# Performance work log

Measured on AMD Instinct MI355X. Metric: run time of the kernel, lower is better.

## Reference

```python
import jax, jax.numpy as jnp
import numpy as np

MARGIN = 0.3

def _cdist(x):
    # pairwise euclidean distances, safe sqrt (zero grad at 0)
    sq = jnp.sum(x * x, axis=1)
    d2 = sq[:, None] + sq[None, :] - 2.0 * (x @ x.T)
    d2 = jnp.maximum(d2, 0.0)
    safe = jnp.where(d2 > 0, d2, 1.0)
    return jnp.where(d2 > 0, jnp.sqrt(safe), 0.0)

def setup_inputs() -> dict:
    key = jax.random.key(0)
    k1, k2 = jax.random.split(key)
    embeddings = jax.random.normal(k1, (4096, 128), dtype=jnp.float32)
    labels = jax.random.randint(k2, (4096,), 0, 256)
    return {"embeddings": embeddings, "labels": labels}

def reference(embeddings, labels):
    B = embeddings.shape[0]
    dist = _cdist(embeddings)                      # [B, B]
    same = labels[:, None] == labels[None, :]      # [B, B]
    eye = jnp.eye(B, dtype=bool)
    pos_mask = same & ~eye
    neg_mask = ~same
    neg_inf = jnp.array(-jnp.inf, dist.dtype)
    pos_inf = jnp.array(jnp.inf, dist.dtype)
    hard_pos = jnp.max(jnp.where(pos_mask, dist, neg_inf), axis=1)  # [B]
    hard_neg = jnp.min(jnp.where(neg_mask, dist, pos_inf), axis=1)  # [B]
    valid = jnp.any(pos_mask, axis=1) & jnp.any(neg_mask, axis=1)
    per_row = jax.nn.relu(hard_pos - hard_neg + MARGIN)
    per_row = jnp.where(valid, per_row, 0.0)
    num_valid = jnp.sum(valid.astype(dist.dtype))
    return jnp.sum(per_row) / jnp.maximum(num_valid, 1.0)
```

## Files before the change

kernel.cpp:

```cpp
#include <hip/hip_runtime.h>
#include <hip/hip_bf16.h>


typedef __attribute__((ext_vector_type(8))) short short8;
typedef __attribute__((ext_vector_type(4))) float f32x4;

#define MARGIN_F 0.3f
#define WST 72

__device__ inline unsigned short f2bf(float x) {
    __hip_bfloat16 h = __float2bfloat16(x);
    return *(unsigned short*)&h;
}
__device__ inline float bf2f(unsigned short u) {
    __hip_bfloat16 h;
    *(unsigned short*)&h = u;
    return __bfloat162float(h);
}

__global__ __launch_bounds__(256) void tl_prep(const float* __restrict__ E,
                                               unsigned short* __restrict__ Ecat,
                                               float* __restrict__ sqn,
                                               unsigned* __restrict__ hpb,
                                               unsigned* __restrict__ hnb) {
    int t = blockIdx.x * 256 + threadIdx.x;
    int row = t >> 5;
    int kq = (t & 31) * 4;
    float4 v = *(const float4*)&E[(size_t)row * 128 + kq];
    float s = fmaf(v.x, v.x, fmaf(v.y, v.y, fmaf(v.z, v.z, v.w * v.w)));

    unsigned short hx = f2bf(v.x), hy = f2bf(v.y), hz = f2bf(v.z), hw = f2bf(v.w);
    unsigned short lx = f2bf(v.x - bf2f(hx)), ly = f2bf(v.y - bf2f(hy));
    unsigned short lz = f2bf(v.z - bf2f(hz)), lw = f2bf(v.w - bf2f(hw));
    ushort4 hi4; hi4.x = hx; hi4.y = hy; hi4.z = hz; hi4.w = hw;
    ushort4 lo4; lo4.x = lx; lo4.y = ly; lo4.z = lz; lo4.w = lw;
    *(ushort4*)&Ecat[(size_t)row * 256 + kq] = hi4;
    *(ushort4*)&Ecat[(size_t)row * 256 + 128 + kq] = lo4;

#pragma unroll
    for (int m = 1; m < 32; m <<= 1) s += __shfl_xor(s, m);
    if ((t & 31) == 0) {
        sqn[row] = s;
        hpb[row] = 0u;
        hnb[row] = 0x7F800000u;
    }
}

__global__ __launch_bounds__(256) void tl_phase1(const unsigned short* __restrict__ Ecat,
                                                 const int* __restrict__ labels,
                                                 const float* __restrict__ sqn,
                                                 unsigned* __restrict__ hpb,
                                                 unsigned* __restrict__ hnb) {
    __shared__ unsigned short Al[128 * WST];
    __shared__ unsigned short Bl[128 * WST];
    const int tid = threadIdx.x;
    const int l = tid & 63, w = tid >> 6;
    const int wr = w >> 1, wc = w & 1;
    const int q = l >> 4, r16 = l & 15;
    const int i0 = blockIdx.x * 128;
    const int jgrp = blockIdx.y * 256;

    float mp[4][4], mn[4][4];
    int li[4][4];
    float si[4][4];
#pragma unroll
    for (int ti = 0; ti < 4; ++ti)
#pragma unroll
        for (int p = 0; p < 4; ++p) {
            mp[ti][p] = 0.0f;
            mn[ti][p] = 3.4e38f;
            int rrow = i0 + wr * 64 + ti * 16 + q * 4 + p;
            li[ti][p] = labels[rrow];
            si[ti][p] = sqn[rrow];
        }

    for (int js = 0; js < 2; ++js) {
        const int jb = jgrp + js * 128;
        f32x4 acc[4][4];
#pragma unroll
        for (int ti = 0; ti < 4; ++ti)
#pragma unroll
            for (int tj = 0; tj < 4; ++tj) acc[ti][tj] = (f32x4)0.0f;

        for (int kc = 0; kc < 4; ++kc) {
            __syncthreads();
#pragma unroll
            for (int it = 0; it < 4; ++it) {
                int idx = it * 256 + tid;
                int rr = idx >> 3, ko = (idx & 7) * 8;
                *(short8*)&Al[rr * WST + ko] =
                    *(const short8*)&Ecat[(size_t)(i0 + rr) * 256 + kc * 64 + ko];
                *(short8*)&Bl[rr * WST + ko] =
                    *(const short8*)&Ecat[(size_t)(jb + rr) * 256 + kc * 64 + ko];
            }
            __syncthreads();
#pragma unroll
            for (int s = 0; s < 2; ++s) {
                short8 af[4], bf[4];
#pragma unroll
                for (int t2 = 0; t2 < 4; ++t2) {
                    af[t2] = *(const short8*)&Al[(wr * 64 + t2 * 16 + r16) * WST + s * 32 + q * 8];
                    bf[t2] = *(const short8*)&Bl[(wc * 64 + t2 * 16 + r16) * WST + s * 32 + q * 8];
                }
#pragma unroll
                for (int ti = 0; ti < 4; ++ti)
#pragma unroll
                    for (int tj = 0; tj < 4; ++tj)
                        acc[ti][tj] = __builtin_amdgcn_mfma_f32_16x16x32_bf16(
                            af[ti], bf[tj], acc[ti][tj], 0, 0, 0);
            }
        }
#pragma unroll
        for (int tj = 0; tj < 4; ++tj) {
            int cj = jb + wc * 64 + tj * 16 + r16;
            int ljv = labels[cj];
            float sjv = sqn[cj];
#pragma unroll
            for (int ti = 0; ti < 4; ++ti) {
#pragma unroll
                for (int p = 0; p < 4; ++p) {
                    float g = acc[ti][tj][p];
                    float d2 = fmaf(-2.0f, g, si[ti][p] + sjv);
                    d2 = fmaxf(d2, 0.0f);
                    int rrow = i0 + wr * 64 + ti * 16 + q * 4 + p;
                    bool same = (li[ti][p] == ljv);
                    bool posok = same && (rrow != cj);
                    mp[ti][p] = fmaxf(mp[ti][p], posok ? d2 : 0.0f);
                    mn[ti][p] = fminf(mn[ti][p], same ? 3.4e38f : d2);
                }
            }
        }
    }
#pragma unroll
    for (int ti = 0; ti < 4; ++ti)
#pragma unroll
        for (int p = 0; p < 4; ++p) {
            float a = mp[ti][p], b = mn[ti][p];
#pragma unroll
            for (int m = 1; m < 16; m <<= 1) {
                a = fmaxf(a, __shfl_xor(a, m));
                b = fminf(b, __shfl_xor(b, m));
            }
            if (r16 == 0) {
                int rrow = i0 + wr * 64 + ti * 16 + q * 4 + p;
                atomicMax(&hpb[rrow], __float_as_uint(a));
                atomicMin(&hnb[rrow], __float_as_uint(b));
            }
        }
}

__global__ __launch_bounds__(1024) void tl_phase2(const int* __restrict__ labels,
                                                  const unsigned* __restrict__ hpb,
                                                  const unsigned* __restrict__ hnb,
                                                  float* __restrict__ out) {
    __shared__ unsigned hist[256];
    __shared__ float sp[16], sv[16];
    int tid = threadIdx.x;
    if (tid < 256) hist[tid] = 0u;
    __syncthreads();
#pragma unroll
    for (int k = 0; k < 4; ++k) atomicAdd(&hist[labels[tid + k * 1024]], 1u);
    __syncthreads();
    float sum = 0.0f, nv = 0.0f;
#pragma unroll
    for (int k = 0; k < 4; ++k) {
        int r = tid + k * 1024;
        unsigned cnt = hist[labels[r]];
        bool valid = (cnt >= 2u) && (cnt < 4096u);
        float hp = sqrtf(__uint_as_float(hpb[r]));
        float hn = sqrtf(__uint_as_float(hnb[r]));
        float pr = fmaxf(hp - hn + MARGIN_F, 0.0f);
        if (valid) { sum += pr; nv += 1.0f; }
    }
#pragma unroll
    for (int m = 1; m < 64; m <<= 1) {
        sum += __shfl_xor(sum, m);
        nv += __shfl_xor(nv, m);
    }
    int wv = tid >> 6;
    if ((tid & 63) == 0) { sp[wv] = sum; sv[wv] = nv; }
    __syncthreads();
    if (tid == 0) {
        float ts = 0.0f, tn = 0.0f;
#pragma unroll
        for (int i = 0; i < 16; ++i) { ts += sp[i]; tn += sv[i]; }
        out[0] = ts / fmaxf(tn, 1.0f);
    }
}

extern "C" void kernel_launch(void* const* d_in, const int* in_sizes, int n_in,
                              void* d_out, int out_size, void* d_ws, size_t ws_size,
                              hipStream_t stream) {
    const float* E = (const float*)d_in[0];
    const int* labels = (const int*)d_in[1];
    float* out = (float*)d_out;

    unsigned short* Ecat = (unsigned short*)d_ws;
    char* base = (char*)d_ws + (size_t)4096 * 256 * 2;
    float* sqn = (float*)base;
    unsigned* hpb = (unsigned*)(base + 16384);
    unsigned* hnb = (unsigned*)(base + 32768);

    tl_prep<<<512, 256, 0, stream>>>(E, Ecat, sqn, hpb, hnb);
    tl_phase1<<<dim3(32, 16), 256, 0, stream>>>(Ecat, labels, sqn, hpb, hnb);
    tl_phase2<<<1, 1024, 0, stream>>>(labels, hpb, hnb, out);
}
```

Measured before the change: 88.15 us.

## Exploit distance-matrix symmetry by computing only upper-triangular tiles

Phase 1 now launches one block per upper-triangular 128x128 tile pair (528 blocks) instead of covering the full matrix with 512 blocks of 128x256. Each off-diagonal tile updates both the row and the column hardest-positive/negative via extra column reductions and atomics. Diagonal tiles reuse the A tile in shared memory as B. This roughly halves the MFMA and load work, at the cost of index math, more atomics and a shorter per-block workload.

Measured after the change: 86.84 us. Within noise of the previous version (-1.5%).

```diff
diff --git a/kernel.cpp b/kernel.cpp
--- a/kernel.cpp
+++ b/kernel.cpp
@@ -53,16 +53,23 @@
                                                  unsigned* __restrict__ hnb) {
     __shared__ unsigned short Al[128 * WST];
     __shared__ unsigned short Bl[128 * WST];
+
+    const int t = blockIdx.x;
+    int bi = (int)((65.0f - sqrtf(4225.0f - 8.0f * (float)t)) * 0.5f);
+    bi = min(max(bi, 0), 31);
+    while (bi < 31 && ((bi + 1) * (65 - (bi + 1))) / 2 <= t) ++bi;
+    while (bi > 0 && (bi * (65 - bi)) / 2 > t) --bi;
+    const int bj = bi + (t - (bi * (65 - bi)) / 2);
+    const bool diag = (bi == bj);
+    const int i0 = bi * 128, j0 = bj * 128;
+
     const int tid = threadIdx.x;
     const int l = tid & 63, w = tid >> 6;
     const int wr = w >> 1, wc = w & 1;
     const int q = l >> 4, r16 = l & 15;
-    const int i0 = blockIdx.x * 128;
-    const int jgrp = blockIdx.y * 256;
-
-    float mp[4][4], mn[4][4];
+
+    float mp[4][4], mn[4][4], si[4][4];
     int li[4][4];
-    float si[4][4];
 #pragma unroll
     for (int ti = 0; ti < 4; ++ti)
 #pragma unroll
@@ -74,60 +81,73 @@
             si[ti][p] = sqn[rrow];
         }
 
-    for (int js = 0; js < 2; ++js) {
-        const int jb = jgrp + js * 128;
-        f32x4 acc[4][4];
-#pragma unroll
-        for (int ti = 0; ti < 4; ++ti)
-#pragma unroll
-            for (int tj = 0; tj < 4; ++tj) acc[ti][tj] = (f32x4)0.0f;
-
-        for (int kc = 0; kc < 4; ++kc) {
-            __syncthreads();
-#pragma unroll
-            for (int it = 0; it < 4; ++it) {
-                int idx = it * 256 + tid;
-                int rr = idx >> 3, ko = (idx & 7) * 8;
-                *(short8*)&Al[rr * WST + ko] =
-                    *(const short8*)&Ecat[(size_t)(i0 + rr) * 256 + kc * 64 + ko];
+    f32x4 acc[4][4];
+#pragma unroll
+    for (int ti = 0; ti < 4; ++ti)
+#pragma unroll
+        for (int tj = 0; tj < 4; ++tj) acc[ti][tj] = (f32x4)0.0f;
+
+    const unsigned short* Bsel = diag ? Al : Bl;
+
+    for (int kc = 0; kc < 4; ++kc) {
+        __syncthreads();
+#pragma unroll
+        for (int it = 0; it < 4; ++it) {
+            int idx = it * 256 + tid;
+            int rr = idx >> 3, ko = (idx & 7) * 8;
+            *(short8*)&Al[rr * WST + ko] =
+                *(const short8*)&Ecat[(size_t)(i0 + rr) * 256 + kc * 64 + ko];
+            if (!diag)
                 *(short8*)&Bl[rr * WST + ko] =
-                    *(const short8*)&Ecat[(size_t)(jb + rr) * 256 + kc * 64 + ko];
-            }
-            __syncthreads();
-#pragma unroll
-            for (int s = 0; s < 2; ++s) {
-                short8 af[4], bf[4];
-#pragma unroll
-                for (int t2 = 0; t2 < 4; ++t2) {
-                    af[t2] = *(const short8*)&Al[(wr * 64 + t2 * 16 + r16) * WST + s * 32 + q * 8];
-                    bf[t2] = *(const short8*)&Bl[(wc * 64 + t2 * 16 + r16) * WST + s * 32 + q * 8];
-                }
-#pragma unroll
-                for (int ti = 0; ti < 4; ++ti)
-#pragma unroll
-                    for (int tj = 0; tj < 4; ++tj)
-                        acc[ti][tj] = __builtin_amdgcn_mfma_f32_16x16x32_bf16(
-                            af[ti], bf[tj], acc[ti][tj], 0, 0, 0);
-            }
-        }
-#pragma unroll
-        for (int tj = 0; tj < 4; ++tj) {
-            int cj = jb + wc * 64 + tj * 16 + r16;
-            int ljv = labels[cj];
-            float sjv = sqn[cj];
-#pragma unroll
-            for (int ti = 0; ti < 4; ++ti) {
-#pragma unroll
-                for (int p = 0; p < 4; ++p) {
-                    float g = acc[ti][tj][p];
-                    float d2 = fmaf(-2.0f, g, si[ti][p] + sjv);
-                    d2 = fmaxf(d2, 0.0f);
-                    int rrow = i0 + wr * 64 + ti * 16 + q * 4 + p;
-                    bool same = (li[ti][p] == ljv);
-                    bool posok = same && (rrow != cj);
-                    mp[ti][p] = fmaxf(mp[ti][p], posok ? d2 : 0.0f);
-                    mn[ti][p] = fminf(mn[ti][p], same ? 3.4e38f : d2);
-                }
+                    *(const short8*)&Ecat[(size_t)(j0 + rr) * 256 + kc * 64 + ko];
+        }
+        __syncthreads();
+#pragma unroll
+        for (int s = 0; s < 2; ++s) {
+            short8 af[4], bf[4];
+#pragma unroll
+            for (int t2 = 0; t2 < 4; ++t2) {
+                af[t2] = *(const short8*)&Al[(wr * 64 + t2 * 16 + r16) * WST + s * 32 + q * 8];
+                bf[t2] = *(const short8*)&Bsel[(wc * 64 + t2 * 16 + r16) * WST + s * 32 + q * 8];
+            }
+#pragma unroll
+            for (int ti = 0; ti < 4; ++ti)
+#pragma unroll
+                for (int tj = 0; tj < 4; ++tj)
+                    acc[ti][tj] = __builtin_amdgcn_mfma_f32_16x16x32_bf16(
+                        af[ti], bf[tj], acc[ti][tj], 0, 0, 0);
+        }
+    }
+
+#pragma unroll
+    for (int tj = 0; tj < 4; ++tj) {
+        int cj = j0 + wc * 64 + tj * 16 + r16;
+        int ljv = labels[cj];
+        float sjv = sqn[cj];
+        float cMP = 0.0f, cMN = 3.4e38f;
+#pragma unroll
+        for (int ti = 0; ti < 4; ++ti) {
+#pragma unroll
+            for (int p = 0; p < 4; ++p) {
+                float g = acc[ti][tj][p];
+                float d2 = fmaxf(fmaf(-2.0f, g, si[ti][p] + sjv), 0.0f);
+                bool same = (li[ti][p] == ljv);
+                int rrow = i0 + wr * 64 + ti * 16 + q * 4 + p;
+                bool self = diag && (rrow == cj);
+                mp[ti][p] = fmaxf(mp[ti][p], (same && !self) ? d2 : 0.0f);
+                mn[ti][p] = fminf(mn[ti][p], same ? 3.4e38f : d2);
+                cMP = fmaxf(cMP, same ? d2 : 0.0f);
+                cMN = fminf(cMN, same ? 3.4e38f : d2);
+            }
+        }
+        if (!diag) {
+            cMP = fmaxf(cMP, __shfl_xor(cMP, 16));
+            cMP = fmaxf(cMP, __shfl_xor(cMP, 32));
+            cMN = fminf(cMN, __shfl_xor(cMN, 16));
+            cMN = fminf(cMN, __shfl_xor(cMN, 32));
+            if (l < 16) {
+                atomicMax(&hpb[cj], __float_as_uint(cMP));
+                atomicMin(&hnb[cj], __float_as_uint(cMN));
             }
         }
     }
@@ -202,6 +222,6 @@
     unsigned* hnb = (unsigned*)(base + 32768);
 
     tl_prep<<<512, 256, 0, stream>>>(E, Ecat, sqn, hpb, hnb);
-    tl_phase1<<<dim3(32, 16), 256, 0, stream>>>(Ecat, labels, sqn, hpb, hnb);
+    tl_phase1<<<528, 256, 0, stream>>>(Ecat, labels, sqn, hpb, hnb);
     tl_phase2<<<1, 1024, 0, stream>>>(labels, hpb, hnb, out);
 }
```

## Use direct global-to-LDS loads with XOR swizzle, split tiles, and drop atomics

Applied to the files above, without the earlier changes.

Phase 1 now gives each block a single 128x128 tile on a 32x32 grid, up from two column tiles per block. It loads operands with global_load_lds into an XOR-swizzled LDS layout instead of going through registers into a padded layout. The per-row sqn add and the self-index comparison move out of the inner epilogue, and per-tile partial max/min are written to scratch buffers instead of global atomics. Phase 2 runs on 16 blocks that reduce these partials and combine results through an atomic counter. The aim is more parallelism, cheaper staging and a shorter epilogue, at the cost of extra partial-buffer traffic and a more complex final reduction.

Measured after the change: 82.17 us. 1.07x faster.

```diff
diff --git a/kernel.cpp b/kernel.cpp
--- a/kernel.cpp
+++ b/kernel.cpp
@@ -6,24 +6,32 @@
 typedef __attribute__((ext_vector_type(4))) float f32x4;
 
 #define MARGIN_F 0.3f
-#define WST 72
+#define NEG_BIG -3.4e38f
+#define POS_BIG 3.4e38f
+
+__device__ __forceinline__ void gl_lds16(const void* g, void* l) {
+    __builtin_amdgcn_global_load_lds(
+        (const __attribute__((address_space(1))) void*)g,
+        (__attribute__((address_space(3))) void*)l, 16, 0, 0);
+}
 
 __device__ inline unsigned short f2bf(float x) {
-    __hip_bfloat16 h = __float2bfloat16(x);
-    return *(unsigned short*)&h;
+    union { __hip_bfloat16 h; unsigned short u; } c;
+    c.h = __float2bfloat16(x);
+    return c.u;
 }
 __device__ inline float bf2f(unsigned short u) {
-    __hip_bfloat16 h;
-    *(unsigned short*)&h = u;
-    return __bfloat162float(h);
+    union { __hip_bfloat16 h; unsigned short us; } c;
+    c.us = u;
+    return __bfloat162float(c.h);
 }
 
 __global__ __launch_bounds__(256) void tl_prep(const float* __restrict__ E,
                                                unsigned short* __restrict__ Ecat,
                                                float* __restrict__ sqn,
-                                               unsigned* __restrict__ hpb,
-                                               unsigned* __restrict__ hnb) {
+                                               unsigned* __restrict__ accum) {
     int t = blockIdx.x * 256 + threadIdx.x;
+    if (t < 4) accum[t] = 0u;
     int row = t >> 5;
     int kq = (t & 31) * 4;
     float4 v = *(const float4*)&E[(size_t)row * 128 + kq];
@@ -39,97 +47,92 @@
 
 #pragma unroll
     for (int m = 1; m < 32; m <<= 1) s += __shfl_xor(s, m);
-    if ((t & 31) == 0) {
-        sqn[row] = s;
-        hpb[row] = 0u;
-        hnb[row] = 0x7F800000u;
-    }
-}
-
-__global__ __launch_bounds__(256) void tl_phase1(const unsigned short* __restrict__ Ecat,
-                                                 const int* __restrict__ labels,
-                                                 const float* __restrict__ sqn,
-                                                 unsigned* __restrict__ hpb,
-                                                 unsigned* __restrict__ hnb) {
-    __shared__ unsigned short Al[128 * WST];
-    __shared__ unsigned short Bl[128 * WST];
+    if ((t & 31) == 0) sqn[row] = s;
+}
+
+__global__ __launch_bounds__(256, 3) void tl_phase1(const unsigned short* __restrict__ Ecat,
+                                                    const int* __restrict__ labels,
+                                                    const float* __restrict__ sqn,
+                                                    float* __restrict__ pmp,
+                                                    float* __restrict__ pmn) {
+    __shared__ __align__(16) unsigned short Al[128 * 64];
+    __shared__ __align__(16) unsigned short Bl[128 * 64];
+    __shared__ float mpS[2][128], mnS[2][128];
+
     const int tid = threadIdx.x;
     const int l = tid & 63, w = tid >> 6;
     const int wr = w >> 1, wc = w & 1;
     const int q = l >> 4, r16 = l & 15;
-    const int i0 = blockIdx.x * 128;
-    const int jgrp = blockIdx.y * 256;
+    const int i0 = blockIdx.x * 128, j0 = blockIdx.y * 128;
+
+    const unsigned short* gA[4];
+    const unsigned short* gB[4];
+#pragma unroll
+    for (int t2 = 0; t2 < 4; ++t2) {
+        int s = w * 256 + t2 * 64 + l;
+        int row = s >> 3, ch = (s & 7) ^ (row & 7);
+        gA[t2] = Ecat + (size_t)(i0 + row) * 256 + ch * 8;
+        gB[t2] = Ecat + (size_t)(j0 + row) * 256 + ch * 8;
+    }
+
+    f32x4 acc[4][4];
+#pragma unroll
+    for (int ti = 0; ti < 4; ++ti)
+#pragma unroll
+        for (int tj = 0; tj < 4; ++tj) acc[ti][tj] = (f32x4)0.0f;
+
+    for (int kc = 0; kc < 4; ++kc) {
+        __syncthreads();
+#pragma unroll
+        for (int t2 = 0; t2 < 4; ++t2) {
+            gl_lds16(gA[t2] + kc * 64, &Al[w * 2048 + t2 * 512]);
+            gl_lds16(gB[t2] + kc * 64, &Bl[w * 2048 + t2 * 512]);
+        }
+        __syncthreads();
+#pragma unroll
+        for (int s = 0; s < 2; ++s) {
+            short8 af[4], bf[4];
+            const int cA = ((s * 4 + q) ^ (r16 & 7)) * 8;
+#pragma unroll
+            for (int t2 = 0; t2 < 4; ++t2) {
+                af[t2] = *(const short8*)&Al[(wr * 64 + t2 * 16 + r16) * 64 + cA];
+                bf[t2] = *(const short8*)&Bl[(wc * 64 + t2 * 16 + r16) * 64 + cA];
+            }
+#pragma unroll
+            for (int ti = 0; ti < 4; ++ti)
+#pragma unroll
+                for (int tj = 0; tj < 4; ++tj)
+                    acc[ti][tj] = __builtin_amdgcn_mfma_f32_16x16x32_bf16(
+                        af[ti], bf[tj], acc[ti][tj], 0, 0, 0);
+        }
+    }
 
     float mp[4][4], mn[4][4];
     int li[4][4];
-    float si[4][4];
 #pragma unroll
     for (int ti = 0; ti < 4; ++ti)
 #pragma unroll
         for (int p = 0; p < 4; ++p) {
-            mp[ti][p] = 0.0f;
-            mn[ti][p] = 3.4e38f;
-            int rrow = i0 + wr * 64 + ti * 16 + q * 4 + p;
-            li[ti][p] = labels[rrow];
-            si[ti][p] = sqn[rrow];
-        }
-
-    for (int js = 0; js < 2; ++js) {
-        const int jb = jgrp + js * 128;
-        f32x4 acc[4][4];
+            mp[ti][p] = NEG_BIG;
+            mn[ti][p] = POS_BIG;
+            li[ti][p] = labels[i0 + wr * 64 + ti * 16 + q * 4 + p];
+        }
+    const bool diagblk = (blockIdx.x == blockIdx.y);
+#pragma unroll
+    for (int tj = 0; tj < 4; ++tj) {
+        int cj = j0 + wc * 64 + tj * 16 + r16;
+        int ljv = labels[cj];
+        float sjv = sqn[cj];
 #pragma unroll
         for (int ti = 0; ti < 4; ++ti)
 #pragma unroll
-            for (int tj = 0; tj < 4; ++tj) acc[ti][tj] = (f32x4)0.0f;
-
-        for (int kc = 0; kc < 4; ++kc) {
-            __syncthreads();
-#pragma unroll
-            for (int it = 0; it < 4; ++it) {
-                int idx = it * 256 + tid;
-                int rr = idx >> 3, ko = (idx & 7) * 8;
-                *(short8*)&Al[rr * WST + ko] =
-                    *(const short8*)&Ecat[(size_t)(i0 + rr) * 256 + kc * 64 + ko];
-                *(short8*)&Bl[rr * WST + ko] =
-                    *(const short8*)&Ecat[(size_t)(jb + rr) * 256 + kc * 64 + ko];
-            }
-            __syncthreads();
-#pragma unroll
-            for (int s = 0; s < 2; ++s) {
-                short8 af[4], bf[4];
-#pragma unroll
-                for (int t2 = 0; t2 < 4; ++t2) {
-                    af[t2] = *(const short8*)&Al[(wr * 64 + t2 * 16 + r16) * WST + s * 32 + q * 8];
-                    bf[t2] = *(const short8*)&Bl[(wc * 64 + t2 * 16 + r16) * WST + s * 32 + q * 8];
-                }
-#pragma unroll
-                for (int ti = 0; ti < 4; ++ti)
-#pragma unroll
-                    for (int tj = 0; tj < 4; ++tj)
-                        acc[ti][tj] = __builtin_amdgcn_mfma_f32_16x16x32_bf16(
-                            af[ti], bf[tj], acc[ti][tj], 0, 0, 0);
-            }
-        }
-#pragma unroll
-        for (int tj = 0; tj < 4; ++tj) {
-            int cj = jb + wc * 64 + tj * 16 + r16;
-            int ljv = labels[cj];
-            float sjv = sqn[cj];
-#pragma unroll
-            for (int ti = 0; ti < 4; ++ti) {
-#pragma unroll
-                for (int p = 0; p < 4; ++p) {
-                    float g = acc[ti][tj][p];
-                    float d2 = fmaf(-2.0f, g, si[ti][p] + sjv);
-                    d2 = fmaxf(d2, 0.0f);
-                    int rrow = i0 + wr * 64 + ti * 16 + q * 4 + p;
-                    bool same = (li[ti][p] == ljv);
-                    bool posok = same && (rrow != cj);
-                    mp[ti][p] = fmaxf(mp[ti][p], posok ? d2 : 0.0f);
-                    mn[ti][p] = fminf(mn[ti][p], same ? 3.4e38f : d2);
-                }
-            }
-        }
+            for (int p = 0; p < 4; ++p) {
+                float val = fmaf(-2.0f, acc[ti][tj][p], sjv);
+                bool same = (li[ti][p] == ljv);
+                bool self = diagblk && ((wr * 64 + ti * 16 + q * 4 + p) == (wc * 64 + tj * 16 + r16));
+                mp[ti][p] = fmaxf(mp[ti][p], (same && !self) ? val : NEG_BIG);
+                mn[ti][p] = fminf(mn[ti][p], same ? POS_BIG : val);
+            }
     }
 #pragma unroll
     for (int ti = 0; ti < 4; ++ti)
@@ -142,49 +145,67 @@
                 b = fminf(b, __shfl_xor(b, m));
             }
             if (r16 == 0) {
-                int rrow = i0 + wr * 64 + ti * 16 + q * 4 + p;
-                atomicMax(&hpb[rrow], __float_as_uint(a));
-                atomicMin(&hnb[rrow], __float_as_uint(b));
-            }
-        }
-}
-
-__global__ __launch_bounds__(1024) void tl_phase2(const int* __restrict__ labels,
-                                                  const unsigned* __restrict__ hpb,
-                                                  const unsigned* __restrict__ hnb,
-                                                  float* __restrict__ out) {
+                int rloc = wr * 64 + ti * 16 + q * 4 + p;
+                mpS[wc][rloc] = a;
+                mnS[wc][rloc] = b;
+            }
+        }
+    __syncthreads();
+    if (tid < 128) {
+        pmp[(size_t)blockIdx.y * 4096 + i0 + tid] = fmaxf(mpS[0][tid], mpS[1][tid]);
+        pmn[(size_t)blockIdx.y * 4096 + i0 + tid] = fminf(mnS[0][tid], mnS[1][tid]);
+    }
+}
+
+__global__ __launch_bounds__(256) void tl_phase2(const int* __restrict__ labels,
+                                                 const float* __restrict__ pmp,
+                                                 const float* __restrict__ pmn,
+                                                 const float* __restrict__ sqn,
+                                                 float* __restrict__ accum,
+                                                 float* __restrict__ out) {
     __shared__ unsigned hist[256];
-    __shared__ float sp[16], sv[16];
+    __shared__ float sp[4], sv[4];
     int tid = threadIdx.x;
-    if (tid < 256) hist[tid] = 0u;
-    __syncthreads();
-#pragma unroll
-    for (int k = 0; k < 4; ++k) atomicAdd(&hist[labels[tid + k * 1024]], 1u);
-    __syncthreads();
-    float sum = 0.0f, nv = 0.0f;
-#pragma unroll
-    for (int k = 0; k < 4; ++k) {
-        int r = tid + k * 1024;
-        unsigned cnt = hist[labels[r]];
-        bool valid = (cnt >= 2u) && (cnt < 4096u);
-        float hp = sqrtf(__uint_as_float(hpb[r]));
-        float hn = sqrtf(__uint_as_float(hnb[r]));
-        float pr = fmaxf(hp - hn + MARGIN_F, 0.0f);
-        if (valid) { sum += pr; nv += 1.0f; }
-    }
+    hist[tid] = 0u;
+    __syncthreads();
+#pragma unroll
+    for (int k = 0; k < 16; ++k) atomicAdd(&hist[labels[k * 256 + tid]], 1u);
+    __syncthreads();
+
+    int r = blockIdx.x * 256 + tid;
+    float mp = NEG_BIG, mn = POS_BIG;
+#pragma unroll
+    for (int k = 0; k < 32; ++k) {
+        mp = fmaxf(mp, pmp[(size_t)k * 4096 + r]);
+        mn = fminf(mn, pmn[(size_t)k * 4096 + r]);
+    }
+    float si = sqn[r];
+    unsigned cnt = hist[labels[r]];
+    bool valid = (cnt >= 2u) && (cnt < 4096u);
+    float hp = sqrtf(fmaxf(si + mp, 0.0f));
+    float hn = sqrtf(fmaxf(si + mn, 0.0f));
+    float pr = fmaxf(hp - hn + MARGIN_F, 0.0f);
+    float s = valid ? pr : 0.0f;
+    float n = valid ? 1.0f : 0.0f;
 #pragma unroll
     for (int m = 1; m < 64; m <<= 1) {
-        sum += __shfl_xor(sum, m);
-        nv += __shfl_xor(nv, m);
-    }
-    int wv = tid >> 6;
-    if ((tid & 63) == 0) { sp[wv] = sum; sv[wv] = nv; }
+        s += __shfl_xor(s, m);
+        n += __shfl_xor(n, m);
+    }
+    if ((tid & 63) == 0) { sp[tid >> 6] = s; sv[tid >> 6] = n; }
     __syncthreads();
     if (tid == 0) {
-        float ts = 0.0f, tn = 0.0f;
-#pragma unroll
-        for (int i = 0; i < 16; ++i) { ts += sp[i]; tn += sv[i]; }
-        out[0] = ts / fmaxf(tn, 1.0f);
+        float ts = sp[0] + sp[1] + sp[2] + sp[3];
+        float tn = sv[0] + sv[1] + sv[2] + sv[3];
+        atomicAdd(&accum[0], ts);
+        atomicAdd(&accum[1], tn);
+        __threadfence();
+        unsigned tk = atomicAdd((unsigned*)&accum[2], 1u);
+        if (tk == 15u) {
+            float a = atomicAdd(&accum[0], 0.0f);
+            float b = atomicAdd(&accum[1], 0.0f);
+            out[0] = a / fmaxf(b, 1.0f);
+        }
     }
 }
 
@@ -195,13 +216,14 @@
     const int* labels = (const int*)d_in[1];
     float* out = (float*)d_out;
 
-    unsigned short* Ecat = (unsigned short*)d_ws;
-    char* base = (char*)d_ws + (size_t)4096 * 256 * 2;
-    float* sqn = (float*)base;
-    unsigned* hpb = (unsigned*)(base + 16384);
-    unsigned* hnb = (unsigned*)(base + 32768);
-
-    tl_prep<<<512, 256, 0, stream>>>(E, Ecat, sqn, hpb, hnb);
-    tl_phase1<<<dim3(32, 16), 256, 0, stream>>>(Ecat, labels, sqn, hpb, hnb);
-    tl_phase2<<<1, 1024, 0, stream>>>(labels, hpb, hnb, out);
-}
+    char* base = (char*)d_ws;
+    unsigned short* Ecat = (unsigned short*)base;
+    float* pmp = (float*)(base + (2u << 20));
+    float* pmn = (float*)(base + (2u << 20) + (512u << 10));
+    float* sqn = (float*)(base + (3u << 20));
+    float* accum = (float*)(base + (3u << 20) + (16u << 10));
+
+    tl_prep<<<512, 256, 0, stream>>>(E, Ecat, sqn, (unsigned*)accum);
+    tl_phase1<<<dim3(32, 32), 256, 0, stream>>>(Ecat, labels, sqn, pmp, pmn);
+    tl_phase2<<<16, 256, 0, stream>>>(labels, pmp, pmn, sqn, accum, out);
+}
```
